# Kernel optimization log

Measured on AMD Instinct MI355X. Metric: run time of the kernel, lower is better.

## Reference

```python
import jax, jax.numpy as jnp
import numpy as np

D_MODEL = 1024
N_HEADS = 16
HEAD_DIM = D_MODEL // N_HEADS


def setup_inputs() -> dict:
    key = jax.random.key(0)
    ks = jax.random.split(key, 5)
    B, S = 2, 2048
    x = jax.random.normal(ks[0], (B, S, D_MODEL), dtype=jnp.float32)
    # nn.Linear weights: [out_features, in_features]
    s_in = 1.0 / np.sqrt(D_MODEL)
    qkv_w = jax.random.uniform(ks[1], (3 * D_MODEL, D_MODEL), jnp.float32, -s_in, s_in)
    qkv_b = jax.random.uniform(ks[2], (3 * D_MODEL,), jnp.float32, -s_in, s_in)
    out_w = jax.random.uniform(ks[3], (D_MODEL, D_MODEL), jnp.float32, -s_in, s_in)
    out_b = jax.random.uniform(ks[4], (D_MODEL,), jnp.float32, -s_in, s_in)
    return {"x": x, "qkv_w": qkv_w, "qkv_b": qkv_b, "out_w": out_w, "out_b": out_b}


def reference(x, qkv_w, qkv_b, out_w, out_b):
    B, S, D = x.shape
    H, Hd = N_HEADS, HEAD_DIM
    scale = 1.0 / np.sqrt(Hd)
    qkv = jnp.einsum('bsd,ed->bse', x, qkv_w) + qkv_b  # [B,S,3D]
    qkv = qkv.reshape(B, S, 3, H, Hd)
    q = qkv[:, :, 0].transpose(0, 2, 1, 3)  # [B,H,S,Hd]
    k = qkv[:, :, 1].transpose(0, 2, 1, 3)
    v = qkv[:, :, 2].transpose(0, 2, 1, 3)
    scores = jnp.einsum('bhqd,bhkd->bhqk', q, k) * scale  # [B,H,S,S]
    causal = jnp.triu(jnp.ones((S, S), dtype=bool), k=1)
    scores = jnp.where(causal[None, None], -jnp.inf, scores)
    probs = jax.nn.softmax(scores, axis=-1)
    out = jnp.einsum('bhqk,bhkd->bhqd', probs, v)  # [B,H,S,Hd]
    out = out.transpose(0, 2, 1, 3).reshape(B, S, D)
    out = jnp.einsum('bsd,ed->bse', out, out_w) + out_b
    return out
```

## Files before the change

kernel.cpp:

```cpp
#include <hip/hip_runtime.h>
#include <hip/hip_bf16.h>

#define SEQ    2048
#define DMODEL 1024
#define NHEAD  16
#define HDIM   64
#define BATCH  2
#define NTOK   (BATCH * SEQ)

#define N_X   (NTOK * DMODEL)
#define N_WQ  (3 * DMODEL * DMODEL)
#define N_BQ  (3 * DMODEL)
#define N_WO  (DMODEL * DMODEL)
#define N_BO  (DMODEL)
#define N_CANON (N_X + N_WQ + N_BQ + N_WO + N_BO)

#define NEG_SENT (-1.0e30f)
#define QSCALE 0.1803368801111f

typedef __attribute__((ext_vector_type(8))) short short8;
typedef __attribute__((ext_vector_type(4))) short short4v;
typedef __attribute__((ext_vector_type(4))) float f32x4;

#define MFMA_BF16(A, B, C) __builtin_amdgcn_mfma_f32_16x16x32_bf16((A), (B), (C), 0, 0, 0)

static __device__ __forceinline__ short8 load8(const __hip_bfloat16* p) {
    return *(const short8*)p;
}

static __device__ __forceinline__ void async16(const void* g, void* l) {
    __builtin_amdgcn_global_load_lds(
        (const __attribute__((address_space(1))) unsigned int*)g,
        (__attribute__((address_space(3))) unsigned int*)l,
        16, 0, 0);
}

__global__ void detect_kernel(const unsigned short* __restrict__ w, int* flag) {
    int cnt = 0;
    for (int i = threadIdx.x; i < 512; i += 64) {
        const unsigned e = (w[i] >> 7) & 0xFF;
        if (e >= 125) cnt++;
    }
#pragma unroll
    for (int o = 32; o; o >>= 1) cnt += __shfl_down(cnt, o);
    if (threadIdx.x == 0) *flag = (cnt > 8) ? 1 : 0;
}

__global__ __launch_bounds__(256) void canon_kernel(
    const void* __restrict__ s0, const void* __restrict__ s1,
    const void* __restrict__ s2, const void* __restrict__ s3,
    const void* __restrict__ s4,
    __hip_bfloat16* __restrict__ dst, const int* __restrict__ flag)
{
    const int v = blockIdx.x * 256 + threadIdx.x;
    if (v >= N_CANON / 8) return;
    const int idx = v * 8;
    const void* src;
    int off;
    if (idx < N_X)                          { src = s0; off = idx; }
    else if (idx < N_X + N_WQ)              { src = s1; off = idx - N_X; }
    else if (idx < N_X + N_WQ + N_BQ)       { src = s2; off = idx - (N_X + N_WQ); }
    else if (idx < N_X + N_WQ + N_BQ + N_WO){ src = s3; off = idx - (N_X + N_WQ + N_BQ); }
    else                                    { src = s4; off = idx - (N_X + N_WQ + N_BQ + N_WO); }
    if (*flag != 0) {
        const f32x4* sp = (const f32x4*)((const float*)src + off);
        const f32x4 x0 = sp[0], x1 = sp[1];
        short8 o;
#pragma unroll
        for (int j = 0; j < 4; ++j) {
            o[j]     = (short)__bfloat16_as_ushort(__float2bfloat16(x0[j]));
            o[4 + j] = (short)__bfloat16_as_ushort(__float2bfloat16(x1[j]));
        }
        *(short8*)&dst[idx] = o;
    } else {
        *(short8*)&dst[idx] = *(const short8*)((const __hip_bfloat16*)src + off);
    }
}

__global__ __launch_bounds__(256) void qkv_gemm_kernel(
    const __hip_bfloat16* __restrict__ X,
    const __hip_bfloat16* __restrict__ W,
    const __hip_bfloat16* __restrict__ bias,
    __hip_bfloat16* __restrict__ Qs,
    __hip_bfloat16* __restrict__ Kb,
    __hip_bfloat16* __restrict__ Vt)
{
    constexpr int Kd = DMODEL;
    __shared__ __align__(16) __hip_bfloat16 As[2][128 * 32];
    __shared__ __align__(16) __hip_bfloat16 Bs[2][128 * 32];

    const int tid   = threadIdx.x;
    const int lane  = tid & 63;
    const int w     = tid >> 6;
    const int mTile = blockIdx.y * 128;
    const int nTile = blockIdx.x * 128;
    const int wm    = (w >> 1) * 64;
    const int wn    = (w & 1) * 64;
    const int lm    = lane & 15;
    const int q4    = lane >> 4;
    const int lks   = (q4 ^ ((lm >> 1) & 3)) * 8;

    f32x4 acc[4][4];
#pragma unroll
    for (int i = 0; i < 4; ++i)
#pragma unroll
        for (int j = 0; j < 4; ++j)
            acc[i][j] = (f32x4){0.f, 0.f, 0.f, 0.f};

    const int r0c = tid >> 2;
    const int r1c = (tid + 256) >> 2;
    const int cbs = ((tid & 3) ^ ((tid >> 3) & 3)) * 8;

    const __hip_bfloat16* gA0 = &X[(size_t)(mTile + r0c) * Kd + cbs];
    const __hip_bfloat16* gA1 = &X[(size_t)(mTile + r1c) * Kd + cbs];
    const __hip_bfloat16* gB0 = &W[(size_t)(nTile + r0c) * Kd + cbs];
    const __hip_bfloat16* gB1 = &W[(size_t)(nTile + r1c) * Kd + cbs];

    async16(gA0, (char*)As[0] + tid * 16);
    async16(gA1, (char*)As[0] + tid * 16 + 4096);
    async16(gB0, (char*)Bs[0] + tid * 16);
    async16(gB1, (char*)Bs[0] + tid * 16 + 4096);

    int cur = 0;
    constexpr int NIT = Kd / 32;
    for (int it = 0; it < NIT; ++it) {
        if (it + 1 < NIT) {
            const int k1 = (it + 1) * 32;
            async16(gA0 + k1, (char*)As[cur ^ 1] + tid * 16);
            async16(gA1 + k1, (char*)As[cur ^ 1] + tid * 16 + 4096);
            async16(gB0 + k1, (char*)Bs[cur ^ 1] + tid * 16);
            async16(gB1 + k1, (char*)Bs[cur ^ 1] + tid * 16 + 4096);
            asm volatile("s_waitcnt vmcnt(4)" ::: "memory");
        } else {
            asm volatile("s_waitcnt vmcnt(0)" ::: "memory");
        }
        __builtin_amdgcn_s_barrier();
        __builtin_amdgcn_sched_barrier(0);

        const __hip_bfloat16* Ac = As[cur];
        const __hip_bfloat16* Bc = Bs[cur];
        short8 a[4], b[4];
#pragma unroll
        for (int i = 0; i < 4; ++i)
            a[i] = *(const short8*)&Ac[(wm + i * 16 + lm) * 32 + lks];
#pragma unroll
        for (int j = 0; j < 4; ++j)
            b[j] = *(const short8*)&Bc[(wn + j * 16 + lm) * 32 + lks];
#pragma unroll
        for (int i = 0; i < 4; ++i)
#pragma unroll
            for (int j = 0; j < 4; ++j)
                acc[i][j] = MFMA_BF16(a[i], b[j], acc[i][j]);

        __builtin_amdgcn_s_barrier();
        cur ^= 1;
    }

    const int r0 = (lane >> 4) * 4;
#pragma unroll
    for (int j = 0; j < 4; ++j) {
        const int n  = nTile + wn + j * 16 + lm;
        const float bv = __bfloat162float(bias[n]);
        const int c = n >> 10;
        const int h = (n >> 6) & 15;
        const int d = n & 63;
#pragma unroll
        for (int i = 0; i < 4; ++i) {
            if (c == 2) {
                const int m0 = mTile + wm + i * 16 + r0;
                const int bb = m0 >> 11;
                const int s0 = m0 & (SEQ - 1);
                const int bh = bb * NHEAD + h;
                short4v pk;
#pragma unroll
                for (int r = 0; r < 4; ++r)
                    pk[r] = (short)__bfloat16_as_ushort(
                        __float2bfloat16(acc[i][j][r] + bv));
                *(short4v*)&Vt[(size_t)(bh * HDIM + d) * SEQ + s0] = pk;
            } else {
#pragma unroll
                for (int r = 0; r < 4; ++r) {
                    const int m  = mTile + wm + i * 16 + r0 + r;
                    const int bb = m >> 11;
                    const int s  = m & (SEQ - 1);
                    const int bh = bb * NHEAD + h;
                    const float v = acc[i][j][r] + bv;
                    if (c == 0) {
                        Qs[(size_t)(bh * SEQ + s) * HDIM + d] = __float2bfloat16(v * QSCALE);
                    } else {
                        Kb[(size_t)(bh * SEQ + s) * HDIM + d] = __float2bfloat16(v);
                    }
                }
            }
        }
    }
}

#define P_PITCH 72
__global__ __launch_bounds__(512, 6) void attn_kernel(
    const __hip_bfloat16* __restrict__ Qs,
    const __hip_bfloat16* __restrict__ Kb,
    const __hip_bfloat16* __restrict__ Vt,
    float* __restrict__ Opart,
    float* __restrict__ MLpart)
{
    __shared__ __align__(16) __hip_bfloat16 Kt[2][64 * 64];
    __shared__ __align__(16) __hip_bfloat16 Vs[2][64 * 64];
    __shared__ __align__(16) __hip_bfloat16 Pall[8][16 * P_PITCH];

    const int tid  = threadIdx.x;
    const int lane = tid & 63;
    const int wv   = tid >> 6;
    const int bh   = blockIdx.x;
    const int py   = blockIdx.y;
    const int p    = py / 3;
    const int j3   = py % 3;

    const int c_lo = (j3 == 0) ? 0 : (j3 == 1 ? 12 : 23);
    const int c_hi = (j3 == 0) ? 12 : (j3 == 1 ? 23 : 34);
    const int bnd  = 32 - 2 * p;

    const int lm  = lane & 15;
    const int q4  = lane >> 4;
    const int lk  = q4 * 8;
    const int swz = (lm & 3) << 4;

    __hip_bfloat16* P = Pall[wv];

    const __hip_bfloat16* Qbh = Qs + (size_t)bh * SEQ * HDIM;
    const __hip_bfloat16* Kbh = Kb + (size_t)bh * SEQ * HDIM;
    const __hip_bfloat16* Vbh = Vt + (size_t)bh * HDIM * SEQ;

    const int srow = tid >> 3;
    const int scb  = (tid & 7) ^ (srow & 7);

    for (int seg = 0; seg < 2; ++seg) {
        int qb, a, b, slot;
        if (seg == 0) {
            if (j3 == 2 && p >= 5) continue;
            qb = 15 - p; a = c_lo;
            b  = (c_hi < bnd) ? c_hi : bnd;
            slot = j3;
        } else {
            if (j3 == 0 || (j3 == 1 && p <= 4)) continue;
            qb = p;
            a  = ((c_lo > bnd) ? c_lo : bnd) - bnd;
            b  = c_hi - bnd;
            slot = (j3 == 2) ? 3 : 4;
        }

        const int wbase = qb * 128 + wv * 16;

        short8 qa[2];
#pragma unroll
        for (int h = 0; h < 2; ++h)
            qa[h] = load8(&Qbh[(size_t)(wbase + lm) * HDIM + h * 32 + lk]);

        float m_run = NEG_SENT;
        float l_run = 0.f;
        f32x4 Oacc[4];
#pragma unroll
        for (int t = 0; t < 4; ++t) Oacc[t] = (f32x4){0.f, 0.f, 0.f, 0.f};

        __builtin_amdgcn_s_barrier();

        {
            const int kk0 = a * 64;
            async16(&Kbh[(size_t)(kk0 + srow) * HDIM + scb * 8], (char*)Kt[0] + tid * 16);
            async16(&Vbh[(size_t)srow * SEQ + kk0 + scb * 8],    (char*)Vs[0] + tid * 16);
            if (a + 1 < b) {
                const int kk1 = kk0 + 64;
                async16(&Kbh[(size_t)(kk1 + srow) * HDIM + scb * 8], (char*)Kt[1] + tid * 16);
                async16(&Vbh[(size_t)srow * SEQ + kk1 + scb * 8],    (char*)Vs[1] + tid * 16);
            }
        }

        int cur = 0;
        for (int ci = a; ci < b; ++ci) {
            const int k0 = ci * 64;

            if (ci + 1 < b) {
                asm volatile("s_waitcnt vmcnt(2)" ::: "memory");
            } else {
                asm volatile("s_waitcnt vmcnt(0)" ::: "memory");
            }
            __builtin_amdgcn_s_barrier();
            __builtin_amdgcn_sched_barrier(0);

            if (k0 <= wbase + 15) {
                const __hip_bfloat16* Kc = Kt[cur];
                const __hip_bfloat16* Vc = Vs[cur];

                short8 ka[4][2];
#pragma unroll
                for (int t = 0; t < 4; ++t)
#pragma unroll
                    for (int h = 0; h < 2; ++h)
                        ka[t][h] = *(const short8*)&Kc[(t * 16 + lm) * 64 +
                                                       (((h * 4 + q4) ^ (lm & 7)) * 8)];

                f32x4 sc[4];
#pragma unroll
                for (int t = 0; t < 4; ++t) sc[t] = (f32x4){0.f, 0.f, 0.f, 0.f};
#pragma unroll
                for (int t = 0; t < 4; ++t) {
                    sc[t] = MFMA_BF16(ka[t][0], qa[0], sc[t]);
                    sc[t] = MFMA_BF16(ka[t][1], qa[1], sc[t]);
                }

                if (k0 + 63 > wbase) {
                    const int row = wbase + lm;
#pragma unroll
                    for (int t = 0; t < 4; ++t)
#pragma unroll
                        for (int r = 0; r < 4; ++r) {
                            const int key = k0 + t * 16 + q4 * 4 + r;
                            if (key > row) sc[t][r] = NEG_SENT;
                        }
                }

                float mx = sc[0][0];
#pragma unroll
                for (int t = 0; t < 4; ++t)
#pragma unroll
                    for (int r = 0; r < 4; ++r) mx = fmaxf(mx, sc[t][r]);
                mx = fmaxf(mx, __shfl_xor(mx, 16));
                mx = fmaxf(mx, __shfl_xor(mx, 32));

                if (!__all(mx <= m_run + 8.0f)) {
                    const float mn = fmaxf(m_run, mx);
                    const float alpha = exp2f(m_run - mn);
                    m_run = mn;
                    l_run *= alpha;
#pragma unroll
                    for (int r = 0; r < 4; ++r) {
                        const float av = __shfl(alpha, q4 * 4 + r);
#pragma unroll
                        for (int t = 0; t < 4; ++t) Oacc[t][r] *= av;
                    }
                }

                float s = 0.f;
#pragma unroll
                for (int t = 0; t < 4; ++t)
#pragma unroll
                    for (int r = 0; r < 4; ++r) {
                        const float pv = exp2f(sc[t][r] - m_run);
                        sc[t][r] = pv;
                        s += pv;
                    }
                s += __shfl_xor(s, 16);
                s += __shfl_xor(s, 32);
                l_run += s;

#pragma unroll
                for (int t = 0; t < 4; ++t) {
                    short4v pk;
#pragma unroll
                    for (int r = 0; r < 4; ++r)
                        pk[r] = (short)__bfloat16_as_ushort(__float2bfloat16(sc[t][r]));
                    const int col = (t * 16 + q4 * 4) ^ swz;
                    *(short4v*)&P[lm * P_PITCH + col] = pk;
                }

#pragma unroll
                for (int h = 0; h < 2; ++h) {
                    const short8 pa = *(const short8*)&P[lm * P_PITCH + ((h * 32 + lk) ^ swz)];
#pragma unroll
                    for (int t = 0; t < 4; ++t) {
                        const short8 vb = *(const short8*)&Vc[(t * 16 + lm) * 64 +
                                                              (((h * 4 + q4) ^ (lm & 7)) * 8)];
                        Oacc[t] = MFMA_BF16(pa, vb, Oacc[t]);
                    }
                }
            }

            __builtin_amdgcn_s_barrier();
            if (ci + 2 < b) {
                const int kk = (ci + 2) * 64;
                async16(&Kbh[(size_t)(kk + srow) * HDIM + scb * 8], (char*)Kt[cur] + tid * 16);
                async16(&Vbh[(size_t)srow * SEQ + kk + scb * 8],    (char*)Vs[cur] + tid * 16);
            }
            cur ^= 1;
        }

        const size_t pbase = ((size_t)(bh * 8 + p) * 5 + slot) * 128;
#pragma unroll
        for (int t = 0; t < 4; ++t)
#pragma unroll
            for (int r = 0; r < 4; ++r)
                Opart[(pbase + wv * 16 + q4 * 4 + r) * 64 + t * 16 + lm] = Oacc[t][r];
        if (lane < 16) {
            MLpart[(pbase + wv * 16 + lane) * 2 + 0] = m_run;
            MLpart[(pbase + wv * 16 + lane) * 2 + 1] = l_run;
        }
    }
}

__global__ __launch_bounds__(256) void attn_merge_kernel(
    const float* __restrict__ Opart, const float* __restrict__ MLpart,
    __hip_bfloat16* __restrict__ O)
{
    const int idx  = blockIdx.x * 256 + threadIdx.x;
    const int d16  = idx & 3;
    const int grow = idx >> 2;
    const int bh   = grow >> 11;
    const int s    = grow & 2047;
    const int qb   = s >> 7;
    const int rin  = s & 127;

    const bool heavy = (qb >= 8);
    const int p  = heavy ? (15 - qb) : qb;
    const int s0 = heavy ? 0 : 3;
    const int s1 = heavy ? 1 : 4;
    const bool v1 = heavy ? true : (p >= 5);
    const bool v2 = heavy && (p <= 4);

    const size_t rb = (size_t)(bh * 8 + p) * 5;
    const size_t r0 = (rb + s0) * 128 + rin;
    const size_t r1 = (rb + s1) * 128 + rin;
    const size_t r2 = (rb + 2)  * 128 + rin;

    const float m0 = MLpart[r0 * 2],                 l0 = MLpart[r0 * 2 + 1];
    const float m1 = v1 ? MLpart[r1 * 2] : NEG_SENT, l1 = v1 ? MLpart[r1 * 2 + 1] : 0.f;
    const float m2 = v2 ? MLpart[r2 * 2] : NEG_SENT, l2 = v2 ? MLpart[r2 * 2 + 1] : 0.f;

    float mm = fmaxf(m0, fmaxf(m1, m2));
    const float a0 = exp2f(m0 - mm);
    const float a1 = v1 ? exp2f(m1 - mm) : 0.f;
    const float a2 = v2 ? exp2f(m2 - mm) : 0.f;
    const float inv = 1.0f / (a0 * l0 + a1 * l1 + a2 * l2);

    f32x4 o[4];
    {
        const f32x4* O0 = (const f32x4*)&Opart[r0 * 64 + d16 * 16];
#pragma unroll
        for (int v = 0; v < 4; ++v) o[v] = a0 * O0[v];
    }
    if (v1) {
        const f32x4* O1 = (const f32x4*)&Opart[r1 * 64 + d16 * 16];
#pragma unroll
        for (int v = 0; v < 4; ++v) o[v] += a1 * O1[v];
    }
    if (v2) {
        const f32x4* O2 = (const f32x4*)&Opart[r2 * 64 + d16 * 16];
#pragma unroll
        for (int v = 0; v < 4; ++v) o[v] += a2 * O2[v];
    }

    short8 out[2];
#pragma unroll
    for (int v = 0; v < 4; ++v)
#pragma unroll
        for (int jj = 0; jj < 4; ++jj)
            out[v >> 1][(v & 1) * 4 + jj] = (short)__bfloat16_as_ushort(
                __float2bfloat16(o[v][jj] * inv));

    const int b = bh >> 4, hh = bh & 15;
    __hip_bfloat16* dst = &O[((size_t)b * SEQ + s) * DMODEL + hh * 64 + d16 * 16];
    ((short8*)dst)[0] = out[0];
    ((short8*)dst)[1] = out[1];
}

__global__ __launch_bounds__(256) void proj_gemm_kernel(
    const __hip_bfloat16* __restrict__ A,
    const __hip_bfloat16* __restrict__ W,
    const __hip_bfloat16* __restrict__ bias,
    void* __restrict__ outv,
    const int* __restrict__ flag)
{
    constexpr int Kd = DMODEL;
    __shared__ __align__(16) __hip_bfloat16 As[2][128 * 32];
    __shared__ __align__(16) __hip_bfloat16 Bs[2][64 * 32];

    const int tid   = threadIdx.x;
    const int lane  = tid & 63;
    const int w     = tid >> 6;
    const int mTile = blockIdx.y * 128;
    const int nTile = blockIdx.x * 64;
    const int wm    = (w >> 1) * 64;
    const int wn    = (w & 1) * 32;
    const int lm    = lane & 15;
    const int q4    = lane >> 4;
    const int lks   = (q4 ^ ((lm >> 1) & 3)) * 8;
    const bool f32out = (*flag != 0);

    f32x4 acc[4][2];
#pragma unroll
    for (int i = 0; i < 4; ++i)
#pragma unroll
        for (int j = 0; j < 2; ++j)
            acc[i][j] = (f32x4){0.f, 0.f, 0.f, 0.f};

    const int r0c = tid >> 2;
    const int r1c = (tid + 256) >> 2;
    const int cbs = ((tid & 3) ^ ((tid >> 3) & 3)) * 8;

    const __hip_bfloat16* gA0 = &A[(size_t)(mTile + r0c) * Kd + cbs];
    const __hip_bfloat16* gA1 = &A[(size_t)(mTile + r1c) * Kd + cbs];
    const __hip_bfloat16* gB0 = &W[(size_t)(nTile + r0c) * Kd + cbs];

    async16(gA0, (char*)As[0] + tid * 16);
    async16(gA1, (char*)As[0] + tid * 16 + 4096);
    async16(gB0, (char*)Bs[0] + tid * 16);

    int cur = 0;
    constexpr int NIT = Kd / 32;
    for (int it = 0; it < NIT; ++it) {
        if (it + 1 < NIT) {
            const int k1 = (it + 1) * 32;
            async16(gA0 + k1, (char*)As[cur ^ 1] + tid * 16);
            async16(gA1 + k1, (char*)As[cur ^ 1] + tid * 16 + 4096);
            async16(gB0 + k1, (char*)Bs[cur ^ 1] + tid * 16);
            asm volatile("s_waitcnt vmcnt(3)" ::: "memory");
        } else {
            asm volatile("s_waitcnt vmcnt(0)" ::: "memory");
        }
        __builtin_amdgcn_s_barrier();
        __builtin_amdgcn_sched_barrier(0);

        const __hip_bfloat16* Ac = As[cur];
        const __hip_bfloat16* Bc = Bs[cur];
        short8 a[4], b[2];
#pragma unroll
        for (int i = 0; i < 4; ++i)
            a[i] = *(const short8*)&Ac[(wm + i * 16 + lm) * 32 + lks];
#pragma unroll
        for (int j = 0; j < 2; ++j)
            b[j] = *(const short8*)&Bc[(wn + j * 16 + lm) * 32 + lks];
#pragma unroll
        for (int i = 0; i < 4; ++i)
#pragma unroll
            for (int j = 0; j < 2; ++j)
                acc[i][j] = MFMA_BF16(a[i], b[j], acc[i][j]);

        __builtin_amdgcn_s_barrier();
        cur ^= 1;
    }

    const int r0 = (lane >> 4) * 4;
#pragma unroll
    for (int j = 0; j < 2; ++j) {
        const int n = nTile + wn + j * 16 + lm;
        const float bv = __bfloat162float(bias[n]);
#pragma unroll
        for (int i = 0; i < 4; ++i) {
#pragma unroll
            for (int r = 0; r < 4; ++r) {
                const size_t m = mTile + wm + i * 16 + r0 + r;
                const float v = acc[i][j][r] + bv;
                if (f32out) ((float*)outv)[m * DMODEL + n] = v;
                else ((__hip_bfloat16*)outv)[m * DMODEL + n] = __float2bfloat16(v);
            }
        }
    }
}

extern "C" void kernel_launch(void* const* d_in, const int* in_sizes, int n_in,
                              void* d_out, int out_size, void* d_ws, size_t ws_size,
                              hipStream_t stream) {
    const size_t OFF_CANON = 256;
    const size_t OFF_QS = OFF_CANON + (size_t)N_CANON * 2;
    const size_t OFF_KB = OFF_QS + (size_t)NTOK * DMODEL * 2;
    const size_t OFF_VT = OFF_KB + (size_t)NTOK * DMODEL * 2;
    const size_t OFF_AO = OFF_VT + (size_t)NTOK * DMODEL * 2;
    const size_t OFF_OP = OFF_AO + (size_t)NTOK * DMODEL * 2;
    const size_t OFF_ML = OFF_OP + (size_t)32 * 8 * 5 * 128 * 64 * 4;

    char* wsb = (char*)d_ws;
    int* flag = (int*)wsb;
    __hip_bfloat16* canon = (__hip_bfloat16*)(wsb + OFF_CANON);
    __hip_bfloat16* Xc = canon;
    __hip_bfloat16* Wq = Xc + N_X;
    __hip_bfloat16* Bq = Wq + N_WQ;
    __hip_bfloat16* Wo = Bq + N_BQ;
    __hip_bfloat16* Bo = Wo + N_WO;
    __hip_bfloat16* Qs = (__hip_bfloat16*)(wsb + OFF_QS);
    __hip_bfloat16* Kb = (__hip_bfloat16*)(wsb + OFF_KB);
    __hip_bfloat16* Vt = (__hip_bfloat16*)(wsb + OFF_VT);
    __hip_bfloat16* Ao = (__hip_bfloat16*)(wsb + OFF_AO);
    float* Opart = (float*)(wsb + OFF_OP);
    float* MLpart = (float*)(wsb + OFF_ML);

    detect_kernel<<<1, 64, 0, stream>>>((const unsigned short*)d_in[1], flag);
    canon_kernel<<<(N_CANON / 8 + 255) / 256, 256, 0, stream>>>(
        d_in[0], d_in[1], d_in[2], d_in[3], d_in[4], canon, flag);

    {
        dim3 grid(3 * DMODEL / 128, NTOK / 128);
        qkv_gemm_kernel<<<grid, 256, 0, stream>>>(Xc, Wq, Bq, Qs, Kb, Vt);
    }
    {
        dim3 grid(BATCH * NHEAD, 24);
        attn_kernel<<<grid, 512, 0, stream>>>(Qs, Kb, Vt, Opart, MLpart);
        attn_merge_kernel<<<(NTOK * NHEAD * 4) / 256, 256, 0, stream>>>(
            Opart, MLpart, Ao);
    }
    {
        dim3 grid(DMODEL / 64, NTOK / 128);
        proj_gemm_kernel<<<grid, 256, 0, stream>>>(Ao, Wo, Bo, d_out, flag);
    }
}
```

Measured before the change: 190.6 us.

## Triple-buffer GEMM k-loops and give each attention wave 32 query rows

```diff
diff --git a/kernel.cpp b/kernel.cpp
--- a/kernel.cpp
+++ b/kernel.cpp
@@ -86,8 +86,8 @@
     __hip_bfloat16* __restrict__ Vt)
 {
     constexpr int Kd = DMODEL;
-    __shared__ __align__(16) __hip_bfloat16 As[2][128 * 32];
-    __shared__ __align__(16) __hip_bfloat16 Bs[2][128 * 32];
+    __shared__ __align__(16) __hip_bfloat16 As[3][128 * 32];
+    __shared__ __align__(16) __hip_bfloat16 Bs[3][128 * 32];
 
     const int tid   = threadIdx.x;
     const int lane  = tid & 63;
@@ -120,16 +120,15 @@
     async16(gA1, (char*)As[0] + tid * 16 + 4096);
     async16(gB0, (char*)Bs[0] + tid * 16);
     async16(gB1, (char*)Bs[0] + tid * 16 + 4096);
+    async16(gA0 + 32, (char*)As[1] + tid * 16);
+    async16(gA1 + 32, (char*)As[1] + tid * 16 + 4096);
+    async16(gB0 + 32, (char*)Bs[1] + tid * 16);
+    async16(gB1 + 32, (char*)Bs[1] + tid * 16 + 4096);
 
     int cur = 0;
     constexpr int NIT = Kd / 32;
     for (int it = 0; it < NIT; ++it) {
         if (it + 1 < NIT) {
-            const int k1 = (it + 1) * 32;
-            async16(gA0 + k1, (char*)As[cur ^ 1] + tid * 16);
-            async16(gA1 + k1, (char*)As[cur ^ 1] + tid * 16 + 4096);
-            async16(gB0 + k1, (char*)Bs[cur ^ 1] + tid * 16);
-            async16(gB1 + k1, (char*)Bs[cur ^ 1] + tid * 16 + 4096);
             asm volatile("s_waitcnt vmcnt(4)" ::: "memory");
         } else {
             asm volatile("s_waitcnt vmcnt(0)" ::: "memory");
@@ -137,6 +136,15 @@
         __builtin_amdgcn_s_barrier();
         __builtin_amdgcn_sched_barrier(0);
 
+        if (it + 2 < NIT) {
+            const int slot = (cur + 2 >= 3) ? cur - 1 : cur + 2;
+            const int k2 = (it + 2) * 32;
+            async16(gA0 + k2, (char*)As[slot] + tid * 16);
+            async16(gA1 + k2, (char*)As[slot] + tid * 16 + 4096);
+            async16(gB0 + k2, (char*)Bs[slot] + tid * 16);
+            async16(gB1 + k2, (char*)Bs[slot] + tid * 16 + 4096);
+        }
+
         const __hip_bfloat16* Ac = As[cur];
         const __hip_bfloat16* Bc = Bs[cur];
         short8 a[4], b[4];
@@ -152,8 +160,7 @@
             for (int j = 0; j < 4; ++j)
                 acc[i][j] = MFMA_BF16(a[i], b[j], acc[i][j]);
 
-        __builtin_amdgcn_s_barrier();
-        cur ^= 1;
+        cur = (cur + 1 == 3) ? 0 : cur + 1;
     }
 
     const int r0 = (lane >> 4) * 4;
@@ -197,7 +204,7 @@
 }
 
 #define P_PITCH 72
-__global__ __launch_bounds__(512, 6) void attn_kernel(
+__global__ __launch_bounds__(256, 3) void attn_kernel(
     const __hip_bfloat16* __restrict__ Qs,
     const __hip_bfloat16* __restrict__ Kb,
     const __hip_bfloat16* __restrict__ Vt,
@@ -206,7 +213,7 @@
 {
     __shared__ __align__(16) __hip_bfloat16 Kt[2][64 * 64];
     __shared__ __align__(16) __hip_bfloat16 Vs[2][64 * 64];
-    __shared__ __align__(16) __hip_bfloat16 Pall[8][16 * P_PITCH];
+    __shared__ __align__(16) __hip_bfloat16 Pall[4][32 * P_PITCH];
 
     const int tid  = threadIdx.x;
     const int lane = tid & 63;
@@ -231,8 +238,8 @@
     const __hip_bfloat16* Kbh = Kb + (size_t)bh * SEQ * HDIM;
     const __hip_bfloat16* Vbh = Vt + (size_t)bh * HDIM * SEQ;
 
-    const int srow = tid >> 3;
-    const int scb  = (tid & 7) ^ (srow & 7);
+    const int srow0 = tid >> 3;
+    const int scb   = (tid & 7) ^ (srow0 & 7);
 
     for (int seg = 0; seg < 2; ++seg) {
         int qb, a, b, slot;
@@ -249,29 +256,37 @@
             slot = (j3 == 2) ? 3 : 4;
         }
 
-        const int wbase = qb * 128 + wv * 16;
-
-        short8 qa[2];
-#pragma unroll
-        for (int h = 0; h < 2; ++h)
-            qa[h] = load8(&Qbh[(size_t)(wbase + lm) * HDIM + h * 32 + lk]);
-
-        float m_run = NEG_SENT;
-        float l_run = 0.f;
-        f32x4 Oacc[4];
-#pragma unroll
-        for (int t = 0; t < 4; ++t) Oacc[t] = (f32x4){0.f, 0.f, 0.f, 0.f};
+        const int wbase = qb * 128 + wv * 32;
+
+        short8 qa[2][2];
+#pragma unroll
+        for (int i = 0; i < 2; ++i)
+#pragma unroll
+            for (int h = 0; h < 2; ++h)
+                qa[i][h] = load8(&Qbh[(size_t)(wbase + i * 16 + lm) * HDIM + h * 32 + lk]);
+
+        float m_run[2] = {NEG_SENT, NEG_SENT};
+        float l_run[2] = {0.f, 0.f};
+        f32x4 Oacc[2][4];
+#pragma unroll
+        for (int i = 0; i < 2; ++i)
+#pragma unroll
+            for (int t = 0; t < 4; ++t) Oacc[i][t] = (f32x4){0.f, 0.f, 0.f, 0.f};
 
         __builtin_amdgcn_s_barrier();
 
         {
             const int kk0 = a * 64;
-            async16(&Kbh[(size_t)(kk0 + srow) * HDIM + scb * 8], (char*)Kt[0] + tid * 16);
-            async16(&Vbh[(size_t)srow * SEQ + kk0 + scb * 8],    (char*)Vs[0] + tid * 16);
+            async16(&Kbh[(size_t)(kk0 + srow0) * HDIM + scb * 8],      (char*)Kt[0] + tid * 16);
+            async16(&Kbh[(size_t)(kk0 + srow0 + 32) * HDIM + scb * 8], (char*)Kt[0] + tid * 16 + 4096);
+            async16(&Vbh[(size_t)srow0 * SEQ + kk0 + scb * 8],         (char*)Vs[0] + tid * 16);
+            async16(&Vbh[(size_t)(srow0 + 32) * SEQ + kk0 + scb * 8],  (char*)Vs[0] + tid * 16 + 4096);
             if (a + 1 < b) {
                 const int kk1 = kk0 + 64;
-                async16(&Kbh[(size_t)(kk1 + srow) * HDIM + scb * 8], (char*)Kt[1] + tid * 16);
-                async16(&Vbh[(size_t)srow * SEQ + kk1 + scb * 8],    (char*)Vs[1] + tid * 16);
+                async16(&Kbh[(size_t)(kk1 + srow0) * HDIM + scb * 8],      (char*)Kt[1] + tid * 16);
+                async16(&Kbh[(size_t)(kk1 + srow0 + 32) * HDIM + scb * 8], (char*)Kt[1] + tid * 16 + 4096);
+                async16(&Vbh[(size_t)srow0 * SEQ + kk1 + scb * 8],         (char*)Vs[1] + tid * 16);
+                async16(&Vbh[(size_t)(srow0 + 32) * SEQ + kk1 + scb * 8],  (char*)Vs[1] + tid * 16 + 4096);
             }
         }
 
@@ -280,14 +295,14 @@
             const int k0 = ci * 64;
 
             if (ci + 1 < b) {
-                asm volatile("s_waitcnt vmcnt(2)" ::: "memory");
+                asm volatile("s_waitcnt vmcnt(4)" ::: "memory");
             } else {
                 asm volatile("s_waitcnt vmcnt(0)" ::: "memory");
             }
             __builtin_amdgcn_s_barrier();
             __builtin_amdgcn_sched_barrier(0);
 
-            if (k0 <= wbase + 15) {
+            if (k0 <= wbase + 31) {
                 const __hip_bfloat16* Kc = Kt[cur];
                 const __hip_bfloat16* Vc = Vs[cur];
 
@@ -299,78 +314,95 @@
                         ka[t][h] = *(const short8*)&Kc[(t * 16 + lm) * 64 +
                                                        (((h * 4 + q4) ^ (lm & 7)) * 8)];
 
-                f32x4 sc[4];
-#pragma unroll
-                for (int t = 0; t < 4; ++t) sc[t] = (f32x4){0.f, 0.f, 0.f, 0.f};
-#pragma unroll
-                for (int t = 0; t < 4; ++t) {
-                    sc[t] = MFMA_BF16(ka[t][0], qa[0], sc[t]);
-                    sc[t] = MFMA_BF16(ka[t][1], qa[1], sc[t]);
-                }
+                f32x4 sc[2][4];
+#pragma unroll
+                for (int i = 0; i < 2; ++i)
+#pragma unroll
+                    for (int t = 0; t < 4; ++t) sc[i][t] = (f32x4){0.f, 0.f, 0.f, 0.f};
+#pragma unroll
+                for (int t = 0; t < 4; ++t)
+#pragma unroll
+                    for (int i = 0; i < 2; ++i) {
+                        sc[i][t] = MFMA_BF16(ka[t][0], qa[i][0], sc[i][t]);
+                        sc[i][t] = MFMA_BF16(ka[t][1], qa[i][1], sc[i][t]);
+                    }
 
                 if (k0 + 63 > wbase) {
-                    const int row = wbase + lm;
-#pragma unroll
-                    for (int t = 0; t < 4; ++t)
-#pragma unroll
-                        for (int r = 0; r < 4; ++r) {
-                            const int key = k0 + t * 16 + q4 * 4 + r;
-                            if (key > row) sc[t][r] = NEG_SENT;
-                        }
-                }
-
-                float mx = sc[0][0];
-#pragma unroll
-                for (int t = 0; t < 4; ++t)
-#pragma unroll
-                    for (int r = 0; r < 4; ++r) mx = fmaxf(mx, sc[t][r]);
-                mx = fmaxf(mx, __shfl_xor(mx, 16));
-                mx = fmaxf(mx, __shfl_xor(mx, 32));
-
-                if (!__all(mx <= m_run + 8.0f)) {
-                    const float mn = fmaxf(m_run, mx);
-                    const float alpha = exp2f(m_run - mn);
-                    m_run = mn;
-                    l_run *= alpha;
-#pragma unroll
-                    for (int r = 0; r < 4; ++r) {
-                        const float av = __shfl(alpha, q4 * 4 + r);
-#pragma unroll
-                        for (int t = 0; t < 4; ++t) Oacc[t][r] *= av;
+#pragma unroll
+                    for (int i = 0; i < 2; ++i) {
+                        const int row = wbase + i * 16 + lm;
+#pragma unroll
+                        for (int t = 0; t < 4; ++t)
+#pragma unroll
+                            for (int r = 0; r < 4; ++r) {
+                                const int key = k0 + t * 16 + q4 * 4 + r;
+                                if (key > row) sc[i][t][r] = NEG_SENT;
+                            }
                     }
                 }
 
-                float s = 0.f;
-#pragma unroll
-                for (int t = 0; t < 4; ++t)
-#pragma unroll
-                    for (int r = 0; r < 4; ++r) {
-                        const float pv = exp2f(sc[t][r] - m_run);
-                        sc[t][r] = pv;
-                        s += pv;
+#pragma unroll
+                for (int i = 0; i < 2; ++i) {
+                    float mx = sc[i][0][0];
+#pragma unroll
+                    for (int t = 0; t < 4; ++t)
+#pragma unroll
+                        for (int r = 0; r < 4; ++r) mx = fmaxf(mx, sc[i][t][r]);
+                    mx = fmaxf(mx, __shfl_xor(mx, 16));
+                    mx = fmaxf(mx, __shfl_xor(mx, 32));
+
+                    if (!__all(mx <= m_run[i] + 8.0f)) {
+                        const float mn = fmaxf(m_run[i], mx);
+                        const float alpha = exp2f(m_run[i] - mn);
+                        m_run[i] = mn;
+                        l_run[i] *= alpha;
+#pragma unroll
+                        for (int r = 0; r < 4; ++r) {
+                            const float av = __shfl(alpha, q4 * 4 + r);
+#pragma unroll
+                            for (int t = 0; t < 4; ++t) Oacc[i][t][r] *= av;
+                        }
                     }
-                s += __shfl_xor(s, 16);
-                s += __shfl_xor(s, 32);
-                l_run += s;
-
-#pragma unroll
-                for (int t = 0; t < 4; ++t) {
-                    short4v pk;
-#pragma unroll
-                    for (int r = 0; r < 4; ++r)
-                        pk[r] = (short)__bfloat16_as_ushort(__float2bfloat16(sc[t][r]));
-                    const int col = (t * 16 + q4 * 4) ^ swz;
-                    *(short4v*)&P[lm * P_PITCH + col] = pk;
+
+                    float s = 0.f;
+#pragma unroll
+                    for (int t = 0; t < 4; ++t)
+#pragma unroll
+                        for (int r = 0; r < 4; ++r) {
+                            const float pv = exp2f(sc[i][t][r] - m_run[i]);
+                            sc[i][t][r] = pv;
+                            s += pv;
+                        }
+                    s += __shfl_xor(s, 16);
+                    s += __shfl_xor(s, 32);
+                    l_run[i] += s;
                 }
 
 #pragma unroll
+                for (int i = 0; i < 2; ++i)
+#pragma unroll
+                    for (int t = 0; t < 4; ++t) {
+                        short4v pk;
+#pragma unroll
+                        for (int r = 0; r < 4; ++r)
+                            pk[r] = (short)__bfloat16_as_ushort(__float2bfloat16(sc[i][t][r]));
+                        const int col = (t * 16 + q4 * 4) ^ swz;
+                        *(short4v*)&P[(i * 16 + lm) * P_PITCH + col] = pk;
+                    }
+
+#pragma unroll
                 for (int h = 0; h < 2; ++h) {
-                    const short8 pa = *(const short8*)&P[lm * P_PITCH + ((h * 32 + lk) ^ swz)];
+                    short8 pa[2];
+#pragma unroll
+                    for (int i = 0; i < 2; ++i)
+                        pa[i] = *(const short8*)&P[(i * 16 + lm) * P_PITCH + ((h * 32 + lk) ^ swz)];
 #pragma unroll
                     for (int t = 0; t < 4; ++t) {
                         const short8 vb = *(const short8*)&Vc[(t * 16 + lm) * 64 +
                                                               (((h * 4 + q4) ^ (lm & 7)) * 8)];
-                        Oacc[t] = MFMA_BF16(pa, vb, Oacc[t]);
+#pragma unroll
+                        for (int i = 0; i < 2; ++i)
+                            Oacc[i][t] = MFMA_BF16(pa[i], vb, Oacc[i][t]);
                     }
                 }
             }
@@ -378,21 +410,28 @@
             __builtin_amdgcn_s_barrier();
             if (ci + 2 < b) {
                 const int kk = (ci + 2) * 64;
-                async16(&Kbh[(size_t)(kk + srow) * HDIM + scb * 8], (char*)Kt[cur] + tid * 16);
-                async16(&Vbh[(size_t)srow * SEQ + kk + scb * 8],    (char*)Vs[cur] + tid * 16);
+                async16(&Kbh[(size_t)(kk + srow0) * HDIM + scb * 8],      (char*)Kt[cur] + tid * 16);
+                async16(&Kbh[(size_t)(kk + srow0 + 32) * HDIM + scb * 8], (char*)Kt[cur] + tid * 16 + 4096);
+                async16(&Vbh[(size_t)srow0 * SEQ + kk + scb * 8],         (char*)Vs[cur] + tid * 16);
+                async16(&Vbh[(size_t)(srow0 + 32) * SEQ + kk + scb * 8],  (char*)Vs[cur] + tid * 16 + 4096);
             }
             cur ^= 1;
         }
 
         const size_t pbase = ((size_t)(bh * 8 + p) * 5 + slot) * 128;
 #pragma unroll
-        for (int t = 0; t < 4; ++t)
-#pragma unroll
-            for (int r = 0; r < 4; ++r)
-                Opart[(pbase + wv * 16 + q4 * 4 + r) * 64 + t * 16 + lm] = Oacc[t][r];
+        for (int i = 0; i < 2; ++i)
+#pragma unroll
+            for (int t = 0; t < 4; ++t)
+#pragma unroll
+                for (int r = 0; r < 4; ++r)
+                    Opart[(pbase + wv * 32 + i * 16 + q4 * 4 + r) * 64 + t * 16 + lm] = Oacc[i][t][r];
         if (lane < 16) {
-            MLpart[(pbase + wv * 16 + lane) * 2 + 0] = m_run;
-            MLpart[(pbase + wv * 16 + lane) * 2 + 1] = l_run;
+#pragma unroll
+            for (int i = 0; i < 2; ++i) {
+                MLpart[(pbase + wv * 32 + i * 16 + lane) * 2 + 0] = m_run[i];
+                MLpart[(pbase + wv * 32 + i * 16 + lane) * 2 + 1] = l_run[i];
+            }
         }
     }
 }
@@ -470,8 +509,8 @@
     const int* __restrict__ flag)
 {
     constexpr int Kd = DMODEL;
-    __shared__ __align__(16) __hip_bfloat16 As[2][128 * 32];
-    __shared__ __align__(16) __hip_bfloat16 Bs[2][64 * 32];
+    __shared__ __align__(16) __hip_bfloat16 As[3][128 * 32];
+    __shared__ __align__(16) __hip_bfloat16 Bs[3][64 * 32];
 
     const int tid   = threadIdx.x;
     const int lane  = tid & 63;
@@ -503,15 +542,14 @@
     async16(gA0, (char*)As[0] + tid * 16);
     async16(gA1, (char*)As[0] + tid * 16 + 4096);
     async16(gB0, (char*)Bs[0] + tid * 16);
+    async16(gA0 + 32, (char*)As[1] + tid * 16);
+    async16(gA1 + 32, (char*)As[1] + tid * 16 + 4096);
+    async16(gB0 + 32, (char*)Bs[1] + tid * 16);
 
     int cur = 0;
     constexpr int NIT = Kd / 32;
     for (int it = 0; it < NIT; ++it) {
         if (it + 1 < NIT) {
-            const int k1 = (it + 1) * 32;
-            async16(gA0 + k1, (char*)As[cur ^ 1] + tid * 16);
-            async16(gA1 + k1, (char*)As[cur ^ 1] + tid * 16 + 4096);
-            async16(gB0 + k1, (char*)Bs[cur ^ 1] + tid * 16);
             asm volatile("s_waitcnt vmcnt(3)" ::: "memory");
         } else {
             asm volatile("s_waitcnt vmcnt(0)" ::: "memory");
@@ -519,6 +557,14 @@
         __builtin_amdgcn_s_barrier();
         __builtin_amdgcn_sched_barrier(0);
 
+        if (it + 2 < NIT) {
+            const int slot = (cur + 2 >= 3) ? cur - 1 : cur + 2;
+            const int k2 = (it + 2) * 32;
+            async16(gA0 + k2, (char*)As[slot] + tid * 16);
+            async16(gA1 + k2, (char*)As[slot] + tid * 16 + 4096);
+            async16(gB0 + k2, (char*)Bs[slot] + tid * 16);
+        }
+
         const __hip_bfloat16* Ac = As[cur];
         const __hip_bfloat16* Bc = Bs[cur];
         short8 a[4], b[2];
@@ -534,8 +580,7 @@
             for (int j = 0; j < 2; ++j)
                 acc[i][j] = MFMA_BF16(a[i], b[j], acc[i][j]);
 
-        __builtin_amdgcn_s_barrier();
-        cur ^= 1;
+        cur = (cur + 1 == 3) ? 0 : cur + 1;
     }
 
     const int r0 = (lane >> 4) * 4;
@@ -592,7 +637,7 @@
     }
     {
         dim3 grid(BATCH * NHEAD, 24);
-        attn_kernel<<<grid, 512, 0, stream>>>(Qs, Kb, Vt, Opart, MLpart);
+        attn_kernel<<<grid, 256, 0, stream>>>(Qs, Kb, Vt, Opart, MLpart);
         attn_merge_kernel<<<(NTOK * NHEAD * 4) / 256, 256, 0, stream>>>(
             Opart, MLpart, Ao);
     }
```

New measurement: 191.6 us. About the same (+0.5%).
